# Kernel tuning notes

Hardware: AMD Instinct MI355X
Metric: run time of the kernel (lower is better)

## Reference

```python
import jax, jax.numpy as jnp
import numpy as np

B, T, D_MODEL, N_HEADS = 2, 2048, 2048, 16
D_HEAD = D_MODEL // N_HEADS
SCALE = 1.0 / np.sqrt(D_HEAD)


def setup_inputs() -> dict:
    key = jax.random.key(0)
    ks = jax.random.split(key, 5)
    w_std = 1.0 / np.sqrt(D_MODEL)
    x = jax.random.normal(ks[0], (B, T, D_MODEL), dtype=jnp.float32)
    W_q = jax.random.normal(ks[1], (D_MODEL, D_MODEL), dtype=jnp.float32) * w_std
    W_k = jax.random.normal(ks[2], (D_MODEL, D_MODEL), dtype=jnp.float32) * w_std
    W_v = jax.random.normal(ks[3], (D_MODEL, D_MODEL), dtype=jnp.float32) * w_std
    W_o = jax.random.normal(ks[4], (D_MODEL, D_MODEL), dtype=jnp.float32) * w_std
    return {"x": x, "W_q": W_q, "W_k": W_k, "W_v": W_v, "W_o": W_o}


def _split_heads(y):
    # [B, T, D] -> [B, H, T, d_head]
    b, t, _ = y.shape
    return y.reshape(b, t, N_HEADS, D_HEAD).transpose(0, 2, 1, 3)


def reference(x, W_q, W_k, W_v, W_o):
    # Linear layers (torch nn.Linear: y = x @ W.T)
    Q = _split_heads(x @ W_q.T)
    K = _split_heads(x @ W_k.T)
    V = _split_heads(x @ W_v.T)
    # Causal softmax attention (math-equivalent to the tiled online-softmax loop)
    scores = jnp.einsum('bhqd,bhkd->bhqk', Q, K) * SCALE
    causal_mask = jnp.tril(jnp.ones((T, T), dtype=bool))  # [T, T]
    scores = jnp.where(causal_mask, scores, -jnp.inf)
    P = jax.nn.softmax(scores, axis=-1)
    O = jnp.einsum('bhqk,bhkd->bhqd', P, V)
    out = O.transpose(0, 2, 1, 3).reshape(B, T, D_MODEL)  # merge heads
    return out @ W_o.T
```

## Files before the change

kernel.cpp:

```cpp
#include <hip/hip_runtime.h>
#include <hip/hip_bf16.h>
#include <hip/hip_fp16.h>

#define B_   2
#define T_   2048
#define DM   2048
#define NH   16
#define DH   128
#define M_   (B_*T_)
#define SCALE_ 0.08838834764831845f

typedef _Float16 f16;
typedef f16  half8 __attribute__((ext_vector_type(8)));
typedef f16  half4 __attribute__((ext_vector_type(4)));
typedef float f32x4 __attribute__((ext_vector_type(4)));

#define GL16(gp, lp) __builtin_amdgcn_global_load_lds( \
    (const __attribute__((address_space(1))) void*)(gp), \
    (__attribute__((address_space(3))) void*)(lp), 16, 0, 0)

#define MFMA16(a, b, c) __builtin_amdgcn_mfma_f32_16x16x32_f16((a), (b), (c), 0, 0, 0)

struct CvtArgs { const float* s[5]; f16* d[5]; };

__global__ __launch_bounds__(256) void convert_all(CvtArgs a) {
    size_t i4 = (size_t)blockIdx.x * 256 + threadIdx.x;
    int r; size_t off;
    if (i4 < 2097152) { r = 0; off = i4; }
    else { size_t k = i4 - 2097152; r = 1 + (int)(k >> 20); off = k & 1048575; }
    float4 v = *((const float4*)a.s[r] + off);
    half4 h;
    h[0] = (f16)v.x; h[1] = (f16)v.y; h[2] = (f16)v.z; h[3] = (f16)v.w;
    *((half4*)a.d[r] + off) = h;
}

#define NT_K 32

__global__ __launch_bounds__(512, 4)
void qkv3(const f16* __restrict__ A, const f16* __restrict__ Bw,
          f16* __restrict__ dst)
{
    __shared__ __align__(16) char smem[81920];

    const int tid  = threadIdx.x;
    const int lane = tid & 63;
    const int w    = tid >> 6;
    const int wr   = w >> 2, wc = w & 3;

    const int id = (blockIdx.x & 7) * 128 + (blockIdx.x >> 3);
    const int bm = id & 31, bn = id >> 5;
    const int m0 = bm * 128, n0 = bn * 192;

    const int scol8 = (((tid & 7) ^ ((tid >> 3) & 7)) << 3);
    const int rc0 = (((lane >> 4) * 16)      ) ^ ((lane & 7) << 4);
    const int rc1 = (64 + (lane >> 4) * 16   ) ^ ((lane & 7) << 4);

    f32x4 acc[4][3] = {};

#define QSTAGE_A(bufb, s, kt) GL16( \
    A + (size_t)(m0 + (tid>>8)*64 + (s)*32 + ((tid>>3)&31)) * 2048 + (kt)*64 + scol8, \
    smem + (bufb)*40960 + (s)*8192 + w*1024)
#define QSTAGE_B(bufb, u, kt) GL16( \
    Bw + (size_t)(n0 + (tid>>7)*48 + (u)*16 + ((tid>>3)&15)) * 2048 + (kt)*64 + scol8, \
    smem + (bufb)*40960 + 16384 + (u)*8192 + w*1024)

    QSTAGE_A(0, 0, 0); QSTAGE_A(0, 1, 0);
    QSTAGE_B(0, 0, 0); QSTAGE_B(0, 1, 0); QSTAGE_B(0, 2, 0);

    const int abase = wr * 4096 + (lane & 15) * 128;
    const int bbase = 16384 + (wc * 16 + (lane & 15)) * 128;

    for (int t = 0; t < NT_K; ++t) {
        const int c  = t & 1;
        const char* buf = smem + c * 40960;
        const int kt = (t + 1 < NT_K) ? t + 1 : t;

        half8 af[4][2], bfr[2];
        asm volatile("s_waitcnt vmcnt(2)" ::: "memory");
        __builtin_amdgcn_s_barrier();
        __builtin_amdgcn_sched_barrier(0);
        #pragma unroll
        for (int m = 0; m < 4; ++m) {
            const char* p = buf + (m >> 1) * 8192 + abase + (m & 1) * 2048;
            af[m][0] = *(const half8*)(p + rc0);
            af[m][1] = *(const half8*)(p + rc1);
        }
        { const char* p = buf + bbase;
          bfr[0] = *(const half8*)(p + rc0); bfr[1] = *(const half8*)(p + rc1); }
        QSTAGE_A(c ^ 1, 0, kt); QSTAGE_A(c ^ 1, 1, kt);
        __builtin_amdgcn_s_setprio(1);
        #pragma unroll
        for (int m = 0; m < 4; ++m) {
            acc[m][0] = MFMA16(af[m][0], bfr[0], acc[m][0]);
            acc[m][0] = MFMA16(af[m][1], bfr[1], acc[m][0]);
        }
        __builtin_amdgcn_s_setprio(0);

        asm volatile("s_waitcnt vmcnt(3)" ::: "memory");
        __builtin_amdgcn_s_barrier();
        __builtin_amdgcn_sched_barrier(0);
        { const char* p = buf + bbase + 8192;
          bfr[0] = *(const half8*)(p + rc0); bfr[1] = *(const half8*)(p + rc1); }
        QSTAGE_B(c ^ 1, 0, kt); QSTAGE_B(c ^ 1, 1, kt);
        __builtin_amdgcn_s_setprio(1);
        #pragma unroll
        for (int m = 0; m < 4; ++m) {
            acc[m][1] = MFMA16(af[m][0], bfr[0], acc[m][1]);
            acc[m][1] = MFMA16(af[m][1], bfr[1], acc[m][1]);
        }
        __builtin_amdgcn_s_setprio(0);

        asm volatile("s_waitcnt vmcnt(4)" ::: "memory");
        __builtin_amdgcn_s_barrier();
        __builtin_amdgcn_sched_barrier(0);
        { const char* p = buf + bbase + 16384;
          bfr[0] = *(const half8*)(p + rc0); bfr[1] = *(const half8*)(p + rc1); }
        QSTAGE_B(c ^ 1, 2, kt);
        __builtin_amdgcn_s_setprio(1);
        #pragma unroll
        for (int m = 0; m < 4; ++m) {
            acc[m][2] = MFMA16(af[m][0], bfr[0], acc[m][2]);
            acc[m][2] = MFMA16(af[m][1], bfr[1], acc[m][2]);
        }
        __builtin_amdgcn_s_setprio(0);
        __builtin_amdgcn_s_barrier();
    }
#undef QSTAGE_A
#undef QSTAGE_B

    asm volatile("s_waitcnt vmcnt(0)" ::: "memory");

    #pragma unroll
    for (int m = 0; m < 4; ++m)
        #pragma unroll
        for (int u = 0; u < 3; ++u)
            #pragma unroll
            for (int j = 0; j < 4; ++j) {
                int row  = m0 + wr * 64 + m * 16 + (lane >> 4) * 4 + j;
                int gcol = n0 + wc * 48 + u * 16 + (lane & 15);
                int sec = gcol >> 11, cic = gcol & 2047;
                int b = row >> 11, tt = row & (T_ - 1);
                int h = cic >> 7, d = cic & 127;
                float cs = (sec == 0) ? SCALE_ : 1.0f;
                dst[(size_t)sec * ((size_t)M_ * 2048) +
                    ((size_t)(b * NH + h) * T_ + tt) * DH + d] = (f16)(acc[m][u][j] * cs);
            }
}

__global__ __launch_bounds__(512, 4)
void wo2(const f16* __restrict__ A, const f16* __restrict__ Bw,
         float* __restrict__ Cf)
{
    __shared__ __align__(16) char smem[65536];

    const int tid  = threadIdx.x;
    const int lane = tid & 63;
    const int w    = tid >> 6;
    const int wr   = w >> 2, wc = w & 3;

    const int id = (blockIdx.x & 7) * 64 + (blockIdx.x >> 3);
    const int bm = id & 31, bn = id >> 5;
    const int m0 = bm * 128, n0 = bn * 128;

    const int scol8 = (((tid & 7) ^ ((tid >> 3) & 7)) << 3);
    const int rc0 = (((lane >> 4) * 16)      ) ^ ((lane & 7) << 4);
    const int rc1 = (64 + (lane >> 4) * 16   ) ^ ((lane & 7) << 4);

    f32x4 acc[4][2] = {};

#define WSTAGE_A(bufb, s, kt) GL16( \
    A + (size_t)(m0 + (tid>>8)*64 + (s)*32 + ((tid>>3)&31)) * 2048 + (kt)*64 + scol8, \
    smem + (bufb)*32768 + (s)*8192 + w*1024)
#define WSTAGE_B(bufb, u, kt) GL16( \
    Bw + (size_t)(n0 + (tid>>7)*32 + (u)*16 + ((tid>>3)&15)) * 2048 + (kt)*64 + scol8, \
    smem + (bufb)*32768 + 16384 + (u)*8192 + w*1024)

    WSTAGE_A(0, 0, 0); WSTAGE_A(0, 1, 0);
    WSTAGE_B(0, 0, 0); WSTAGE_B(0, 1, 0);

    const int abase = wr * 4096 + (lane & 15) * 128;
    const int bbase = 16384 + (wc * 16 + (lane & 15)) * 128;

    for (int t = 0; t < NT_K; ++t) {
        const int c  = t & 1;
        const char* buf = smem + c * 32768;
        const int kt = (t + 1 < NT_K) ? t + 1 : t;

        half8 af[4][2], bfr[2];
        asm volatile("s_waitcnt vmcnt(1)" ::: "memory");
        __builtin_amdgcn_s_barrier();
        __builtin_amdgcn_sched_barrier(0);
        #pragma unroll
        for (int m = 0; m < 4; ++m) {
            const char* p = buf + (m >> 1) * 8192 + abase + (m & 1) * 2048;
            af[m][0] = *(const half8*)(p + rc0);
            af[m][1] = *(const half8*)(p + rc1);
        }
        { const char* p = buf + bbase;
          bfr[0] = *(const half8*)(p + rc0); bfr[1] = *(const half8*)(p + rc1); }
        WSTAGE_A(c ^ 1, 0, kt); WSTAGE_A(c ^ 1, 1, kt);
        __builtin_amdgcn_s_setprio(1);
        #pragma unroll
        for (int m = 0; m < 4; ++m) {
            acc[m][0] = MFMA16(af[m][0], bfr[0], acc[m][0]);
            acc[m][0] = MFMA16(af[m][1], bfr[1], acc[m][0]);
        }
        __builtin_amdgcn_s_setprio(0);

        asm volatile("s_waitcnt vmcnt(2)" ::: "memory");
        __builtin_amdgcn_s_barrier();
        __builtin_amdgcn_sched_barrier(0);
        { const char* p = buf + bbase + 8192;
          bfr[0] = *(const half8*)(p + rc0); bfr[1] = *(const half8*)(p + rc1); }
        WSTAGE_B(c ^ 1, 0, kt); WSTAGE_B(c ^ 1, 1, kt);
        __builtin_amdgcn_s_setprio(1);
        #pragma unroll
        for (int m = 0; m < 4; ++m) {
            acc[m][1] = MFMA16(af[m][0], bfr[0], acc[m][1]);
            acc[m][1] = MFMA16(af[m][1], bfr[1], acc[m][1]);
        }
        __builtin_amdgcn_s_setprio(0);
        __builtin_amdgcn_s_barrier();
    }
#undef WSTAGE_A
#undef WSTAGE_B

    asm volatile("s_waitcnt vmcnt(0)" ::: "memory");

    #pragma unroll
    for (int m = 0; m < 4; ++m)
        #pragma unroll
        for (int u = 0; u < 2; ++u)
            #pragma unroll
            for (int j = 0; j < 4; ++j) {
                int row = m0 + wr * 64 + m * 16 + (lane >> 4) * 4 + j;
                int col = n0 + wc * 32 + u * 16 + (lane & 15);
                Cf[(size_t)row * 2048 + col] = acc[m][u][j];
            }
}

__global__ __launch_bounds__(256)
void vtrans(const f16* __restrict__ Vin, f16* __restrict__ Vout)
{
    __shared__ f16 ld[64][72];
    const int tid = threadIdx.x;
    const int dd = blockIdx.x;
    const int tt = blockIdx.y;
    const int bh = blockIdx.z;

    const int r  = tid >> 2;
    const int s2 = (tid & 3) * 2;

    const f16* src = Vin + ((size_t)bh * T_ + tt * 64 + r) * DH + dd * 64;
    half8 v0 = *(const half8*)(src + s2 * 8);
    half8 v1 = *(const half8*)(src + s2 * 8 + 8);
    #pragma unroll
    for (int e = 0; e < 8; ++e) ld[s2 * 8 + e][r]     = v0[e];
    #pragma unroll
    for (int e = 0; e < 8; ++e) ld[s2 * 8 + 8 + e][r] = v1[e];
    __syncthreads();

    f16* dst = Vout + ((size_t)bh * DH + dd * 64 + r) * T_ + tt * 64;
    *(half8*)(dst + s2 * 8)     = *(const half8*)&ld[r][s2 * 8];
    *(half8*)(dst + s2 * 8 + 8) = *(const half8*)&ld[r][s2 * 8 + 8];
}

#define QB 64
#define KB 64
#define PP 72
#define NQT (T_/QB)

__global__ __launch_bounds__(256, 4)
void attn_fwd(const f16* __restrict__ Q, const f16* __restrict__ K,
              const f16* __restrict__ Vt, f16* __restrict__ O)
{
    __shared__ __align__(16) char Ks[2][16384];
    __shared__ __align__(16) char Vs[2][16384];
    __shared__ __align__(16) f16 Ps[4][16][PP];

    const int tid  = threadIdx.x;
    const int lane = tid & 63;
    const int w    = tid >> 6;
    const int g    = lane >> 4;

    const int bid  = blockIdx.x;
    const int swz  = (bid & 7) * 64 + (bid >> 3);
    const int bh   = swz >> 4;
    const int pair = swz & 15;
    const size_t base = (size_t)bh * T_ * DH;
    const int b = bh >> 4, h = bh & 15;

    const int krow0 = w * 4 + g;
    const int kswz  = ((lane & 15) ^ (krow0 & 7)) << 3;
    const int vrow0 = w * 8 + (lane >> 3);
    const int vswz  = (((lane & 7) ^ ((lane >> 3) & 7)) << 3);

#define STAGE_K(c_, kv) do { \
    _Pragma("unroll") for (int i_ = 0; i_ < 4; ++i_) { \
        const f16* g_ = K + base + (size_t)((kv) + i_*16 + krow0) * DH + kswz; \
        GL16(g_, &Ks[c_][i_*4096 + w*1024]); } } while (0)
#define STAGE_V(c_, kv) do { \
    _Pragma("unroll") for (int i_ = 0; i_ < 4; ++i_) { \
        const f16* g_ = Vt + base + (size_t)(i_*32 + vrow0) * T_ + (kv) + vswz; \
        GL16(g_, &Vs[c_][i_*4096 + w*1024]); } } while (0)

    #pragma unroll
    for (int hf = 0; hf < 2; ++hf) {
        const int qt = (hf == 0) ? pair : (NQT - 1 - pair);
        const int q0 = qt * QB;
        const int ntiles = qt + 1;
        const int qg = q0 + w * 16 + (lane & 15);

        half8 qf[4];
        #pragma unroll
        for (int kk = 0; kk < 4; ++kk)
            qf[kk] = *reinterpret_cast<const half8*>(
                &Q[base + (size_t)qg * DH + kk * 32 + g * 8]);

        float mrun = -1e30f, lrun = 0.f;
        f32x4 o[8] = {};

        __syncthreads();
        STAGE_K(0, 0);
        STAGE_V(0, 0);

        for (int it = 0; it < ntiles; ++it) {
            const int c = it & 1;
            __syncthreads();
            if (it + 1 < ntiles) {
                STAGE_K(c ^ 1, (it + 1) * KB);
                STAGE_V(c ^ 1, (it + 1) * KB);
            }

            const char* kb = &Ks[c][0];
            f32x4 sacc[4] = {};
            __builtin_amdgcn_s_setprio(1);
            #pragma unroll
            for (int n = 0; n < 4; ++n)
                #pragma unroll
                for (int kk = 0; kk < 4; ++kk) {
                    half8 kfv = *(const half8*)(kb + (n*16 + (lane & 15)) * 256 +
                        ((kk*32 + g * 8) * 2 ^ ((lane & 7) << 4)));
                    sacc[n] = MFMA16(kfv, qf[kk], sacc[n]);
                }
            __builtin_amdgcn_s_setprio(0);

            if (it == ntiles - 1) {
                #pragma unroll
                for (int n = 0; n < 4; ++n)
                    #pragma unroll
                    for (int j = 0; j < 4; ++j) {
                        int kg = it * KB + n*16 + g*4 + j;
                        if (kg > qg) sacc[n][j] = -1e30f;
                    }
            }

            float mx = sacc[0][0];
            #pragma unroll
            for (int n = 0; n < 4; ++n)
                #pragma unroll
                for (int j = 0; j < 4; ++j) mx = fmaxf(mx, sacc[n][j]);
            mx = fmaxf(mx, __shfl_xor(mx, 16));
            mx = fmaxf(mx, __shfl_xor(mx, 32));
            float mnew = fmaxf(mrun, mx);
            float sf = __expf(mrun - mnew);
            float rs = 0.f;
            #pragma unroll
            for (int n = 0; n < 4; ++n)
                #pragma unroll
                for (int j = 0; j < 4; ++j) {
                    float p = __expf(sacc[n][j] - mnew);
                    sacc[n][j] = p;
                    rs += p;
                }
            rs += __shfl_xor(rs, 16);
            rs += __shfl_xor(rs, 32);
            lrun = lrun * sf + rs;
            mrun = mnew;
            #pragma unroll
            for (int nn = 0; nn < 8; ++nn) o[nn] *= sf;

            #pragma unroll
            for (int n = 0; n < 4; ++n) {
                half4 hv;
                hv[0] = (f16)sacc[n][0]; hv[1] = (f16)sacc[n][1];
                hv[2] = (f16)sacc[n][2]; hv[3] = (f16)sacc[n][3];
                *reinterpret_cast<half4*>(&Ps[w][lane & 15][n*16 + g*4]) = hv;
            }

            half8 bp[2];
            #pragma unroll
            for (int cc = 0; cc < 2; ++cc)
                bp[cc] = *reinterpret_cast<const half8*>(&Ps[w][lane & 15][cc*32 + g*8]);

            const char* vb = &Vs[c][0];
            __builtin_amdgcn_s_setprio(1);
            #pragma unroll
            for (int n = 0; n < 8; ++n)
                #pragma unroll
                for (int cc = 0; cc < 2; ++cc) {
                    half8 vf = *(const half8*)(vb + (n*16 + (lane & 15)) * 128 +
                        ((cc*64 + g*16) ^ ((lane & 7) << 4)));
                    o[n] = MFMA16(vf, bp[cc], o[n]);
                }
            __builtin_amdgcn_s_setprio(0);
        }

        float invl = 1.0f / lrun;
        #pragma unroll
        for (int n = 0; n < 8; ++n) {
            half4 hv;
            hv[0] = (f16)(o[n][0] * invl); hv[1] = (f16)(o[n][1] * invl);
            hv[2] = (f16)(o[n][2] * invl); hv[3] = (f16)(o[n][3] * invl);
            *reinterpret_cast<half4*>(
                &O[((size_t)(b * T_ + qg) * NH + h) * DH + n*16 + g*4]) = hv;
        }
    }
#undef STAGE_K
#undef STAGE_V
}

extern "C" void kernel_launch(void* const* d_in, const int* in_sizes, int n_in,
                              void* d_out, int out_size, void* d_ws, size_t ws_size,
                              hipStream_t stream)
{
    const float* x  = (const float*)d_in[0];
    const float* wq = (const float*)d_in[1];
    const float* wk = (const float*)d_in[2];
    const float* wv = (const float*)d_in[3];
    const float* wo = (const float*)d_in[4];
    float* out = (float*)d_out;

    const size_t nx = (size_t)M_ * DM;
    const size_t nw = (size_t)DM * DM;
    const size_t need = (nx * 5 + nw * 4) * sizeof(f16);
    if (ws_size < need) return;

    char* ws = (char*)d_ws;
    f16* xh  = (f16*)ws;  ws += nx * 2;
    f16* wqh = (f16*)ws;  ws += nw * 2;
    f16* wkh = (f16*)ws;  ws += nw * 2;
    f16* wvh = (f16*)ws;  ws += nw * 2;
    f16* woh = (f16*)ws;  ws += nw * 2;
    f16* Qh  = (f16*)ws;  ws += nx * 2;
    f16* Kh  = (f16*)ws;  ws += nx * 2;
    f16* Vh  = (f16*)ws;  ws += nx * 2;
    f16* Oh  = (f16*)ws;  ws += nx * 2;

    f16* Vth = xh;

    CvtArgs ca;
    ca.s[0] = x;  ca.d[0] = xh;
    ca.s[1] = wq; ca.d[1] = wqh;
    ca.s[2] = wk; ca.d[2] = wkh;
    ca.s[3] = wv; ca.d[3] = wvh;
    ca.s[4] = wo; ca.d[4] = woh;
    convert_all<<<24576, 256, 0, stream>>>(ca);

    qkv3<<<dim3(1024), 512, 0, stream>>>(xh, wqh, Qh);

    vtrans<<<dim3(2, 32, 32), 256, 0, stream>>>(Vh, Vth);

    attn_fwd<<<dim3(512), 256, 0, stream>>>(Qh, Kh, Vth, Oh);

    wo2<<<dim3(512), 512, 0, stream>>>(Oh, woh, out);
}
```

Baseline: 244.5 us.

## Enlarge QKV GEMM block tile to 256x192 with 4x2 warp layout

```diff
diff --git a/kernel.cpp b/kernel.cpp
--- a/kernel.cpp
+++ b/kernel.cpp
@@ -36,46 +36,48 @@
 
 #define NT_K 32
 
-__global__ __launch_bounds__(512, 4)
+__global__ __launch_bounds__(512, 2)
 void qkv3(const f16* __restrict__ A, const f16* __restrict__ Bw,
           f16* __restrict__ dst)
 {
-    __shared__ __align__(16) char smem[81920];
+    __shared__ __align__(16) char smem[114688];
 
     const int tid  = threadIdx.x;
     const int lane = tid & 63;
     const int w    = tid >> 6;
-    const int wr   = w >> 2, wc = w & 3;
-
-    const int id = (blockIdx.x & 7) * 128 + (blockIdx.x >> 3);
-    const int bm = id & 31, bn = id >> 5;
-    const int m0 = bm * 128, n0 = bn * 192;
+    const int wr   = w >> 1, wc = w & 1;
+
+    const int id = (blockIdx.x & 7) * 64 + (blockIdx.x >> 3);
+    const int bm = id & 15, bn = id >> 4;
+    const int m0 = bm * 256, n0 = bn * 192;
 
     const int scol8 = (((tid & 7) ^ ((tid >> 3) & 7)) << 3);
     const int rc0 = (((lane >> 4) * 16)      ) ^ ((lane & 7) << 4);
     const int rc1 = (64 + (lane >> 4) * 16   ) ^ ((lane & 7) << 4);
 
-    f32x4 acc[4][3] = {};
-
-#define QSTAGE_A(bufb, s, kt) GL16( \
-    A + (size_t)(m0 + (tid>>8)*64 + (s)*32 + ((tid>>3)&31)) * 2048 + (kt)*64 + scol8, \
-    smem + (bufb)*40960 + (s)*8192 + w*1024)
+    f32x4 acc[4][6] = {};
+
+#define QSTAGE_A(bufb, ch, s, kt) GL16( \
+    A + (size_t)(m0 + (ch)*128 + (tid>>8)*64 + (s)*32 + ((tid>>3)&31)) * 2048 + (kt)*64 + scol8, \
+    smem + (bufb)*57344 + (ch)*16384 + (s)*8192 + w*1024)
 #define QSTAGE_B(bufb, u, kt) GL16( \
     Bw + (size_t)(n0 + (tid>>7)*48 + (u)*16 + ((tid>>3)&15)) * 2048 + (kt)*64 + scol8, \
-    smem + (bufb)*40960 + 16384 + (u)*8192 + w*1024)
-
-    QSTAGE_A(0, 0, 0); QSTAGE_A(0, 1, 0);
-    QSTAGE_B(0, 0, 0); QSTAGE_B(0, 1, 0); QSTAGE_B(0, 2, 0);
-
-    const int abase = wr * 4096 + (lane & 15) * 128;
-    const int bbase = 16384 + (wc * 16 + (lane & 15)) * 128;
+    smem + (bufb)*57344 + 32768 + (u)*8192 + w*1024)
+
+    QSTAGE_A(0, 0, 0, 0); QSTAGE_A(0, 0, 1, 0);
+    QSTAGE_A(0, 1, 0, 0); QSTAGE_A(0, 1, 1, 0);
+    QSTAGE_B(0, 0, 0);    QSTAGE_B(0, 1, 0);    QSTAGE_B(0, 2, 0);
+
+    const int abase = (wr >> 1) * 16384 + (wr & 1) * 4096 + (lane & 15) * 128;
+    const int bbase = 32768 + wc * 4096 + (lane & 15) * 128;
 
     for (int t = 0; t < NT_K; ++t) {
         const int c  = t & 1;
-        const char* buf = smem + c * 40960;
+        const char* buf = smem + c * 57344;
         const int kt = (t + 1 < NT_K) ? t + 1 : t;
 
-        half8 af[4][2], bfr[2];
+        half8 af[4][2];
+
         asm volatile("s_waitcnt vmcnt(2)" ::: "memory");
         __builtin_amdgcn_s_barrier();
         __builtin_amdgcn_sched_barrier(0);
@@ -85,45 +87,88 @@
             af[m][0] = *(const half8*)(p + rc0);
             af[m][1] = *(const half8*)(p + rc1);
         }
-        { const char* p = buf + bbase;
-          bfr[0] = *(const half8*)(p + rc0); bfr[1] = *(const half8*)(p + rc1); }
-        QSTAGE_A(c ^ 1, 0, kt); QSTAGE_A(c ^ 1, 1, kt);
-        __builtin_amdgcn_s_setprio(1);
-        #pragma unroll
-        for (int m = 0; m < 4; ++m) {
-            acc[m][0] = MFMA16(af[m][0], bfr[0], acc[m][0]);
-            acc[m][0] = MFMA16(af[m][1], bfr[1], acc[m][0]);
-        }
-        __builtin_amdgcn_s_setprio(0);
-
-        asm volatile("s_waitcnt vmcnt(3)" ::: "memory");
+        {
+            const char* p = buf + bbase;
+            half8 b0 = *(const half8*)(p + rc0), b1 = *(const half8*)(p + rc1);
+            QSTAGE_A(c ^ 1, 0, 0, kt); QSTAGE_A(c ^ 1, 0, 1, kt);
+            __builtin_amdgcn_s_setprio(1);
+            #pragma unroll
+            for (int m = 0; m < 4; ++m) {
+                acc[m][0] = MFMA16(af[m][0], b0, acc[m][0]);
+                acc[m][0] = MFMA16(af[m][1], b1, acc[m][0]);
+            }
+            __builtin_amdgcn_s_setprio(0);
+        }
+
+        {
+            const char* p = buf + bbase + 2048;
+            half8 b0 = *(const half8*)(p + rc0), b1 = *(const half8*)(p + rc1);
+            QSTAGE_A(c ^ 1, 1, 0, kt); QSTAGE_A(c ^ 1, 1, 1, kt);
+            __builtin_amdgcn_s_setprio(1);
+            #pragma unroll
+            for (int m = 0; m < 4; ++m) {
+                acc[m][3] = MFMA16(af[m][0], b0, acc[m][3]);
+                acc[m][3] = MFMA16(af[m][1], b1, acc[m][3]);
+            }
+            __builtin_amdgcn_s_setprio(0);
+        }
+
+        asm volatile("s_waitcnt vmcnt(5)" ::: "memory");
         __builtin_amdgcn_s_barrier();
         __builtin_amdgcn_sched_barrier(0);
-        { const char* p = buf + bbase + 8192;
-          bfr[0] = *(const half8*)(p + rc0); bfr[1] = *(const half8*)(p + rc1); }
-        QSTAGE_B(c ^ 1, 0, kt); QSTAGE_B(c ^ 1, 1, kt);
-        __builtin_amdgcn_s_setprio(1);
-        #pragma unroll
-        for (int m = 0; m < 4; ++m) {
-            acc[m][1] = MFMA16(af[m][0], bfr[0], acc[m][1]);
-            acc[m][1] = MFMA16(af[m][1], bfr[1], acc[m][1]);
-        }
-        __builtin_amdgcn_s_setprio(0);
-
-        asm volatile("s_waitcnt vmcnt(4)" ::: "memory");
+        {
+            const char* p = buf + bbase + 8192;
+            half8 b0 = *(const half8*)(p + rc0), b1 = *(const half8*)(p + rc1);
+            QSTAGE_B(c ^ 1, 0, kt);
+            __builtin_amdgcn_s_setprio(1);
+            #pragma unroll
+            for (int m = 0; m < 4; ++m) {
+                acc[m][1] = MFMA16(af[m][0], b0, acc[m][1]);
+                acc[m][1] = MFMA16(af[m][1], b1, acc[m][1]);
+            }
+            __builtin_amdgcn_s_setprio(0);
+        }
+
+        {
+            const char* p = buf + bbase + 8192 + 2048;
+            half8 b0 = *(const half8*)(p + rc0), b1 = *(const half8*)(p + rc1);
+            QSTAGE_B(c ^ 1, 1, kt);
+            __builtin_amdgcn_s_setprio(1);
+            #pragma unroll
+            for (int m = 0; m < 4; ++m) {
+                acc[m][4] = MFMA16(af[m][0], b0, acc[m][4]);
+                acc[m][4] = MFMA16(af[m][1], b1, acc[m][4]);
+            }
+            __builtin_amdgcn_s_setprio(0);
+        }
+
+        asm volatile("s_waitcnt vmcnt(6)" ::: "memory");
         __builtin_amdgcn_s_barrier();
         __builtin_amdgcn_sched_barrier(0);
-        { const char* p = buf + bbase + 16384;
-          bfr[0] = *(const half8*)(p + rc0); bfr[1] = *(const half8*)(p + rc1); }
-        QSTAGE_B(c ^ 1, 2, kt);
-        __builtin_amdgcn_s_setprio(1);
-        #pragma unroll
-        for (int m = 0; m < 4; ++m) {
-            acc[m][2] = MFMA16(af[m][0], bfr[0], acc[m][2]);
-            acc[m][2] = MFMA16(af[m][1], bfr[1], acc[m][2]);
-        }
-        __builtin_amdgcn_s_setprio(0);
-        __builtin_amdgcn_s_barrier();
+        {
+            const char* p = buf + bbase + 16384;
+            half8 b0 = *(const half8*)(p + rc0), b1 = *(const half8*)(p + rc1);
+            QSTAGE_B(c ^ 1, 2, kt);
+            __builtin_amdgcn_s_setprio(1);
+            #pragma unroll
+            for (int m = 0; m < 4; ++m) {
+                acc[m][2] = MFMA16(af[m][0], b0, acc[m][2]);
+                acc[m][2] = MFMA16(af[m][1], b1, acc[m][2]);
+            }
+            __builtin_amdgcn_s_setprio(0);
+        }
+
+        {
+            const char* p = buf + bbase + 16384 + 2048;
+            half8 b0 = *(const half8*)(p + rc0), b1 = *(const half8*)(p + rc1);
+            __builtin_amdgcn_s_setprio(1);
+            #pragma unroll
+            for (int m = 0; m < 4; ++m) {
+                acc[m][5] = MFMA16(af[m][0], b0, acc[m][5]);
+                acc[m][5] = MFMA16(af[m][1], b1, acc[m][5]);
+            }
+            __builtin_amdgcn_s_setprio(0);
+        }
     }
 #undef QSTAGE_A
 #undef QSTAGE_B
@@ -133,17 +178,17 @@
     #pragma unroll
     for (int m = 0; m < 4; ++m)
         #pragma unroll
-        for (int u = 0; u < 3; ++u)
+        for (int f = 0; f < 6; ++f)
             #pragma unroll
             for (int j = 0; j < 4; ++j) {
                 int row  = m0 + wr * 64 + m * 16 + (lane >> 4) * 4 + j;
-                int gcol = n0 + wc * 48 + u * 16 + (lane & 15);
+                int gcol = n0 + wc * 96 + f * 16 + (lane & 15);
                 int sec = gcol >> 11, cic = gcol & 2047;
                 int b = row >> 11, tt = row & (T_ - 1);
                 int h = cic >> 7, d = cic & 127;
                 float cs = (sec == 0) ? SCALE_ : 1.0f;
                 dst[(size_t)sec * ((size_t)M_ * 2048) +
-                    ((size_t)(b * NH + h) * T_ + tt) * DH + d] = (f16)(acc[m][u][j] * cs);
+                    ((size_t)(b * NH + h) * T_ + tt) * DH + d] = (f16)(acc[m][f][j] * cs);
             }
 }
 
@@ -457,7 +502,7 @@
     ca.s[4] = wo; ca.d[4] = woh;
     convert_all<<<24576, 256, 0, stream>>>(ca);
 
-    qkv3<<<dim3(1024), 512, 0, stream>>>(xh, wqh, Qh);
+    qkv3<<<dim3(512), 512, 0, stream>>>(xh, wqh, Qh);
 
     vtrans<<<dim3(2, 32, 32), 256, 0, stream>>>(Vh, Vth);
 
```

Measured after the change: 242.6 us. About the same (-0.8%).

## Retile QKV GEMM to 256x128 blocks with K=32 steps and simpler pipeline

Applied to the files above, without the earlier changes.

```diff
diff --git a/kernel.cpp b/kernel.cpp
--- a/kernel.cpp
+++ b/kernel.cpp
@@ -34,118 +34,86 @@
     *((half4*)a.d[r] + off) = h;
 }
 
-#define NT_K 32
+#define NTQ 64
 
 __global__ __launch_bounds__(512, 4)
 void qkv3(const f16* __restrict__ A, const f16* __restrict__ Bw,
           f16* __restrict__ dst)
 {
-    __shared__ __align__(16) char smem[81920];
+    __shared__ __align__(16) char smem[49152];
 
     const int tid  = threadIdx.x;
     const int lane = tid & 63;
     const int w    = tid >> 6;
-    const int wr   = w >> 2, wc = w & 3;
-
-    const int id = (blockIdx.x & 7) * 128 + (blockIdx.x >> 3);
-    const int bm = id & 31, bn = id >> 5;
-    const int m0 = bm * 128, n0 = bn * 192;
-
-    const int scol8 = (((tid & 7) ^ ((tid >> 3) & 7)) << 3);
-    const int rc0 = (((lane >> 4) * 16)      ) ^ ((lane & 7) << 4);
-    const int rc1 = (64 + (lane >> 4) * 16   ) ^ ((lane & 7) << 4);
-
-    f32x4 acc[4][3] = {};
-
-#define QSTAGE_A(bufb, s, kt) GL16( \
-    A + (size_t)(m0 + (tid>>8)*64 + (s)*32 + ((tid>>3)&31)) * 2048 + (kt)*64 + scol8, \
-    smem + (bufb)*40960 + (s)*8192 + w*1024)
-#define QSTAGE_B(bufb, u, kt) GL16( \
-    Bw + (size_t)(n0 + (tid>>7)*48 + (u)*16 + ((tid>>3)&15)) * 2048 + (kt)*64 + scol8, \
-    smem + (bufb)*40960 + 16384 + (u)*8192 + w*1024)
-
-    QSTAGE_A(0, 0, 0); QSTAGE_A(0, 1, 0);
-    QSTAGE_B(0, 0, 0); QSTAGE_B(0, 1, 0); QSTAGE_B(0, 2, 0);
-
-    const int abase = wr * 4096 + (lane & 15) * 128;
-    const int bbase = 16384 + (wc * 16 + (lane & 15)) * 128;
-
-    for (int t = 0; t < NT_K; ++t) {
-        const int c  = t & 1;
-        const char* buf = smem + c * 40960;
-        const int kt = (t + 1 < NT_K) ? t + 1 : t;
-
-        half8 af[4][2], bfr[2];
-        asm volatile("s_waitcnt vmcnt(2)" ::: "memory");
+    const int wr   = w >> 1, wc = w & 1;
+
+    const int id = (blockIdx.x & 7) * 96 + (blockIdx.x >> 3);
+    const int bm = id & 15, bn = id >> 4;
+    const int m0 = bm * 256, n0 = bn * 128;
+
+    const int scol8 = (((tid & 3) ^ ((tid >> 2) & 3)) << 3);
+    const int rca = (lane & 15) * 64 + ((((lane >> 4) ^ lane) & 3) << 4);
+
+    f32x4 acc[4][4] = {};
+
+#define QA(bufb, s, kt) GL16( \
+    A + (size_t)(m0 + (s)*128 + (tid>>2)) * 2048 + (kt)*32 + scol8, \
+    smem + (bufb)*24576 + (s)*8192 + w*1024)
+#define QB(bufb, kt) GL16( \
+    Bw + (size_t)(n0 + (tid>>2)) * 2048 + (kt)*32 + scol8, \
+    smem + (bufb)*24576 + 16384 + w*1024)
+
+    QA(0, 0, 0); QA(0, 1, 0); QB(0, 0);
+
+    for (int t = 0; t < NTQ; ++t) {
+        const int c = t & 1;
+        const char* buf = smem + c * 24576;
+
+        asm volatile("s_waitcnt vmcnt(0)" ::: "memory");
         __builtin_amdgcn_s_barrier();
         __builtin_amdgcn_sched_barrier(0);
-        #pragma unroll
-        for (int m = 0; m < 4; ++m) {
-            const char* p = buf + (m >> 1) * 8192 + abase + (m & 1) * 2048;
-            af[m][0] = *(const half8*)(p + rc0);
-            af[m][1] = *(const half8*)(p + rc1);
-        }
-        { const char* p = buf + bbase;
-          bfr[0] = *(const half8*)(p + rc0); bfr[1] = *(const half8*)(p + rc1); }
-        QSTAGE_A(c ^ 1, 0, kt); QSTAGE_A(c ^ 1, 1, kt);
+
+        if (t + 1 < NTQ) {
+            QA(c ^ 1, 0, t + 1); QA(c ^ 1, 1, t + 1); QB(c ^ 1, t + 1);
+        }
+
+        half8 af[4], bf[4];
+        #pragma unroll
+        for (int m = 0; m < 4; ++m)
+            af[m] = *(const half8*)(buf + wr * 4096 + m * 1024 + rca);
+        #pragma unroll
+        for (int n = 0; n < 4; ++n)
+            bf[n] = *(const half8*)(buf + 16384 + wc * 4096 + n * 1024 + rca);
+
         __builtin_amdgcn_s_setprio(1);
         #pragma unroll
-        for (int m = 0; m < 4; ++m) {
-            acc[m][0] = MFMA16(af[m][0], bfr[0], acc[m][0]);
-            acc[m][0] = MFMA16(af[m][1], bfr[1], acc[m][0]);
-        }
+        for (int m = 0; m < 4; ++m)
+            #pragma unroll
+            for (int n = 0; n < 4; ++n)
+                acc[m][n] = MFMA16(af[m], bf[n], acc[m][n]);
         __builtin_amdgcn_s_setprio(0);
-
-        asm volatile("s_waitcnt vmcnt(3)" ::: "memory");
-        __builtin_amdgcn_s_barrier();
-        __builtin_amdgcn_sched_barrier(0);
-        { const char* p = buf + bbase + 8192;
-          bfr[0] = *(const half8*)(p + rc0); bfr[1] = *(const half8*)(p + rc1); }
-        QSTAGE_B(c ^ 1, 0, kt); QSTAGE_B(c ^ 1, 1, kt);
-        __builtin_amdgcn_s_setprio(1);
-        #pragma unroll
-        for (int m = 0; m < 4; ++m) {
-            acc[m][1] = MFMA16(af[m][0], bfr[0], acc[m][1]);
-            acc[m][1] = MFMA16(af[m][1], bfr[1], acc[m][1]);
-        }
-        __builtin_amdgcn_s_setprio(0);
-
-        asm volatile("s_waitcnt vmcnt(4)" ::: "memory");
-        __builtin_amdgcn_s_barrier();
-        __builtin_amdgcn_sched_barrier(0);
-        { const char* p = buf + bbase + 16384;
-          bfr[0] = *(const half8*)(p + rc0); bfr[1] = *(const half8*)(p + rc1); }
-        QSTAGE_B(c ^ 1, 2, kt);
-        __builtin_amdgcn_s_setprio(1);
-        #pragma unroll
-        for (int m = 0; m < 4; ++m) {
-            acc[m][2] = MFMA16(af[m][0], bfr[0], acc[m][2]);
-            acc[m][2] = MFMA16(af[m][1], bfr[1], acc[m][2]);
-        }
-        __builtin_amdgcn_s_setprio(0);
-        __builtin_amdgcn_s_barrier();
     }
-#undef QSTAGE_A
-#undef QSTAGE_B
-
-    asm volatile("s_waitcnt vmcnt(0)" ::: "memory");
+#undef QA
+#undef QB
 
     #pragma unroll
     for (int m = 0; m < 4; ++m)
         #pragma unroll
-        for (int u = 0; u < 3; ++u)
+        for (int n = 0; n < 4; ++n)
             #pragma unroll
             for (int j = 0; j < 4; ++j) {
                 int row  = m0 + wr * 64 + m * 16 + (lane >> 4) * 4 + j;
-                int gcol = n0 + wc * 48 + u * 16 + (lane & 15);
+                int gcol = n0 + wc * 64 + n * 16 + (lane & 15);
                 int sec = gcol >> 11, cic = gcol & 2047;
                 int b = row >> 11, tt = row & (T_ - 1);
                 int h = cic >> 7, d = cic & 127;
                 float cs = (sec == 0) ? SCALE_ : 1.0f;
                 dst[(size_t)sec * ((size_t)M_ * 2048) +
-                    ((size_t)(b * NH + h) * T_ + tt) * DH + d] = (f16)(acc[m][u][j] * cs);
+                    ((size_t)(b * NH + h) * T_ + tt) * DH + d] = (f16)(acc[m][n][j] * cs);
             }
 }
+
+#define NT_K 32
 
 __global__ __launch_bounds__(512, 4)
 void wo2(const f16* __restrict__ A, const f16* __restrict__ Bw,
@@ -457,7 +425,7 @@
     ca.s[4] = wo; ca.d[4] = woh;
     convert_all<<<24576, 256, 0, stream>>>(ca);
 
-    qkv3<<<dim3(1024), 512, 0, stream>>>(xh, wqh, Qh);
+    qkv3<<<dim3(768), 512, 0, stream>>>(xh, wqh, Qh);
 
     vtrans<<<dim3(2, 32, 32), 256, 0, stream>>>(Vh, Vth);
 
```

New measurement: 256.7 us. 5.0% more time.
